# Kernel tuning notes

Measured on AMD Instinct MI355X. Metric: run time of the kernel, lower is better.

The kernel has to match this reference:

```python
import jax, jax.numpy as jnp
import numpy as np

VOCAB = 50257
EMB = 100
BOT = 5  # bottleneck dim of the tiny autoencoder MLP


def setup_inputs() -> dict:
    key = jax.random.key(0)
    ks = jax.random.split(key, 7)
    B, S = 128, 2048
    x = jax.random.randint(ks[0], (B, S), 0, VOCAB, dtype=jnp.int64)
    word_embed = jax.random.normal(ks[1], (VOCAB, EMB), dtype=jnp.float32)
    # idf values are positive; use uniform(0,1] scaled up a bit to mimic log-idf
    idf = jax.random.uniform(ks[2], (VOCAB,), dtype=jnp.float32, minval=0.01, maxval=10.0)
    fc1_w = jax.random.normal(ks[3], (BOT, EMB), dtype=jnp.float32) * (1.0 / np.sqrt(EMB))
    fc1_b = jax.random.normal(ks[4], (BOT,), dtype=jnp.float32) * 0.01
    fc2_w = jax.random.normal(ks[5], (EMB, BOT), dtype=jnp.float32) * (1.0 / np.sqrt(BOT))
    fc2_b = jax.random.normal(ks[6], (EMB,), dtype=jnp.float32) * 0.01
    return {"x": x, "word_embed": word_embed, "idf": idf,
            "fc1_w": fc1_w, "fc1_b": fc1_b, "fc2_w": fc2_w, "fc2_b": fc2_b}


def reference(x, word_embed, idf, fc1_w, fc1_b, fc2_w, fc2_b):
    B, S = x.shape
    V = idf.shape[0]
    # tf(): per-row token histogram. Equivalent math to the torch dense
    # one-hot scatter + sum over seq, done as a scatter-add (no (B,S,V) tensor).
    rows = jnp.broadcast_to(jnp.arange(B)[:, None], (B, S))
    tf = jnp.zeros((B, V), dtype=jnp.float32).at[rows, x].add(1.0)
    # tf-idf weights, row-normalized
    tfidf = tf * idf[None, :]
    tfidf = tfidf / jnp.sum(tfidf, axis=1, keepdims=True)
    # per-token weight: gather each row's tfidf at its token ids  -> [B, S]
    w = jnp.take_along_axis(tfidf, x, axis=1)
    # embedding lookup and tfidf-weighted sum over seq  -> [B, EMB]
    emb = word_embed[x]  # [B, S, EMB]
    doc = jnp.einsum('bse,bs->be', emb, w)
    # tiny 100 -> 5 -> 100 MLP (no nonlinearity in the original)
    h = doc @ fc1_w.T + fc1_b
    out = h @ fc2_w.T + fc2_b
    return out
```

## Files before the change

### kernel.cpp

```cpp
#include <hip/hip_runtime.h>

#define SEQ 2048
#define EMB 100
#define BOT 5
#define HSIZE 4096
#define SPLIT 16
#define CHUNK (SEQ / SPLIT)
#define K1T 1024

__global__ __launch_bounds__(K1T) void k1_hist(
    const int* __restrict__ x, const float* __restrict__ idf,
    float* __restrict__ coef)
{
    __shared__ int   hkey[HSIZE];
    __shared__ int   hcnt[HSIZE];
    __shared__ float red[K1T / 64];
    __shared__ float zinv;

    const int b = blockIdx.x, tid = threadIdx.x;
    const int lane = tid & 63, wid = tid >> 6;

    for (int i = tid; i < HSIZE; i += K1T) { hkey[i] = -1; hcnt[i] = 0; }
    __syncthreads();

    const int* xrow = x + (size_t)b * SEQ;

    int   mykey[SEQ / K1T];
    float myidf[SEQ / K1T];
    float z = 0.0f;
    #pragma unroll
    for (int j = 0; j < SEQ / K1T; ++j) {
        int s   = tid + j * K1T;
        int key = xrow[s];
        float w = idf[key];
        mykey[j] = key;
        myidf[j] = w;
        z += w;
        unsigned slot = ((unsigned)key * 2654435761u) >> 20;
        for (;;) {
            int prev = atomicCAS(&hkey[slot], -1, key);
            if (prev == -1 || prev == key) { atomicAdd(&hcnt[slot], 1); break; }
            slot = (slot + 1) & (HSIZE - 1);
        }
    }
    for (int off = 32; off > 0; off >>= 1) z += __shfl_down(z, off);
    if (lane == 0) red[wid] = z;
    __syncthreads();
    if (tid == 0) {
        float t = 0.0f;
        #pragma unroll
        for (int i = 0; i < K1T / 64; ++i) t += red[i];
        zinv = 1.0f / t;
    }
    __syncthreads();
    const float iz = zinv;

    #pragma unroll
    for (int j = 0; j < SEQ / K1T; ++j) {
        int s   = tid + j * K1T;
        int key = mykey[j];
        unsigned slot = ((unsigned)key * 2654435761u) >> 20;
        while (hkey[slot] != key) slot = (slot + 1) & (HSIZE - 1);
        coef[(size_t)b * SEQ + s] = (float)hcnt[slot] * myidf[j] * iz;
    }
}

__global__ __launch_bounds__(256) void k2_gather(
    const int* __restrict__ x, const float* __restrict__ coef,
    const float* __restrict__ we, float* __restrict__ partial)
{
    __shared__ int   skey[CHUNK];
    __shared__ float scoef[CHUNK];
    __shared__ float part[4][EMB];

    const int bx   = blockIdx.x;
    const int b    = bx >> 4;
    const int sp   = bx & (SPLIT - 1);
    const int tid  = threadIdx.x;
    const int wave = tid >> 6;
    const int lane = tid & 63;

    const int base = sp * CHUNK;
    if (tid < CHUNK) {
        skey [tid] = x   [(size_t)b * SEQ + base + tid];
        scoef[tid] = coef[(size_t)b * SEQ + base + tid];
    }
    __syncthreads();

    if (lane < EMB / 2) {
        float2 a0 = {0,0}, a1 = {0,0}, a2 = {0,0}, a3 = {0,0};
        float2 a4 = {0,0}, a5 = {0,0}, a6 = {0,0}, a7 = {0,0};
        const int t0 = wave * 32;
        #pragma unroll
        for (int it = 0; it < 4; ++it) {
            const int i = t0 + it * 8;
            int   k0 = skey[i+0], k1 = skey[i+1], k2 = skey[i+2], k3 = skey[i+3];
            int   k4 = skey[i+4], k5 = skey[i+5], k6 = skey[i+6], k7 = skey[i+7];
            float c0 = scoef[i+0], c1 = scoef[i+1], c2 = scoef[i+2], c3 = scoef[i+3];
            float c4 = scoef[i+4], c5 = scoef[i+5], c6 = scoef[i+6], c7 = scoef[i+7];
            float2 v0 = ((const float2*)(we + (size_t)k0 * EMB))[lane];
            float2 v1 = ((const float2*)(we + (size_t)k1 * EMB))[lane];
            float2 v2 = ((const float2*)(we + (size_t)k2 * EMB))[lane];
            float2 v3 = ((const float2*)(we + (size_t)k3 * EMB))[lane];
            float2 v4 = ((const float2*)(we + (size_t)k4 * EMB))[lane];
            float2 v5 = ((const float2*)(we + (size_t)k5 * EMB))[lane];
            float2 v6 = ((const float2*)(we + (size_t)k6 * EMB))[lane];
            float2 v7 = ((const float2*)(we + (size_t)k7 * EMB))[lane];
            a0.x += c0 * v0.x; a0.y += c0 * v0.y;
            a1.x += c1 * v1.x; a1.y += c1 * v1.y;
            a2.x += c2 * v2.x; a2.y += c2 * v2.y;
            a3.x += c3 * v3.x; a3.y += c3 * v3.y;
            a4.x += c4 * v4.x; a4.y += c4 * v4.y;
            a5.x += c5 * v5.x; a5.y += c5 * v5.y;
            a6.x += c6 * v6.x; a6.y += c6 * v6.y;
            a7.x += c7 * v7.x; a7.y += c7 * v7.y;
        }
        float sx = ((a0.x + a1.x) + (a2.x + a3.x)) + ((a4.x + a5.x) + (a6.x + a7.x));
        float sy = ((a0.y + a1.y) + (a2.y + a3.y)) + ((a4.y + a5.y) + (a6.y + a7.y));
        part[wave][2 * lane]     = sx;
        part[wave][2 * lane + 1] = sy;
    }
    __syncthreads();
    if (tid < EMB)
        partial[(size_t)bx * EMB + tid] =
            (part[0][tid] + part[1][tid]) + (part[2][tid] + part[3][tid]);
}

__global__ __launch_bounds__(128) void k3_mlp(
    const float* __restrict__ partial,
    const float* __restrict__ fc1w, const float* __restrict__ fc1b,
    const float* __restrict__ fc2w, const float* __restrict__ fc2b,
    float* __restrict__ out)
{
    __shared__ float doc[EMB];
    __shared__ float hsh[BOT];

    const int b = blockIdx.x, tid = threadIdx.x;

    if (tid < EMB) {
        float a = 0.0f;
        const float* p = partial + (size_t)b * SPLIT * EMB + tid;
        #pragma unroll
        for (int s = 0; s < SPLIT; ++s) a += p[s * EMB];
        doc[tid] = a;
    }
    __syncthreads();

    if (tid < BOT) {
        float h = fc1b[tid];
        const float* wr = fc1w + tid * EMB;
        for (int e = 0; e < EMB; ++e) h += doc[e] * wr[e];
        hsh[tid] = h;
    }
    __syncthreads();

    if (tid < EMB) {
        float o = fc2b[tid];
        const float* wr = fc2w + tid * BOT;
        #pragma unroll
        for (int j = 0; j < BOT; ++j) o += hsh[j] * wr[j];
        out[(size_t)b * EMB + tid] = o;
    }
}

extern "C" void kernel_launch(void* const* d_in, const int* in_sizes, int n_in,
                              void* d_out, int out_size, void* d_ws, size_t ws_size,
                              hipStream_t stream) {
    const int*   x    = (const int*)d_in[0];
    const float* we   = (const float*)d_in[1];
    const float* idf  = (const float*)d_in[2];
    const float* fc1w = (const float*)d_in[3];
    const float* fc1b = (const float*)d_in[4];
    const float* fc2w = (const float*)d_in[5];
    const float* fc2b = (const float*)d_in[6];
    float*       out  = (float*)d_out;

    const int B = in_sizes[0] / SEQ;

    char* ws = (char*)d_ws;
    float* coef    = (float*)ws;
    float* partial = (float*)(ws + (size_t)B * SEQ * 4);

    k1_hist  <<<B,         K1T, 0, stream>>>(x, idf, coef);
    k2_gather<<<B * SPLIT, 256, 0, stream>>>(x, coef, we, partial);
    k3_mlp   <<<B,         128, 0, stream>>>(partial, fc1w, fc1b, fc2w, fc2b, out);
}
```

Baseline: 103.3 us.

## Fuse MLP into gather via last-block counter; cache hash slots

Removes the third kernel launch. The last of the split blocks for each batch row, detected with an atomic counter that the histogram kernel resets, now reduces the partial sums and runs the small MLP. The histogram kernel also keeps the probed hash slot per token in registers, so it no longer re-probes the table in its second pass. The fusion adds thread fences and an atomic per block in exchange for one fewer launch and no inter-kernel gap.

New measurement: 349.2 us. 3.38x slower.

```diff
diff --git a/kernel.cpp b/kernel.cpp
--- a/kernel.cpp
+++ b/kernel.cpp
@@ -10,7 +10,7 @@
 
 __global__ __launch_bounds__(K1T) void k1_hist(
     const int* __restrict__ x, const float* __restrict__ idf,
-    float* __restrict__ coef)
+    float* __restrict__ coef, int* __restrict__ cnt)
 {
     __shared__ int   hkey[HSIZE];
     __shared__ int   hcnt[HSIZE];
@@ -20,12 +20,13 @@
     const int b = blockIdx.x, tid = threadIdx.x;
     const int lane = tid & 63, wid = tid >> 6;
 
+    if (tid == 0) cnt[b] = 0;
     for (int i = tid; i < HSIZE; i += K1T) { hkey[i] = -1; hcnt[i] = 0; }
     __syncthreads();
 
     const int* xrow = x + (size_t)b * SEQ;
 
-    int   mykey[SEQ / K1T];
+    int   myslot[SEQ / K1T];
     float myidf[SEQ / K1T];
     float z = 0.0f;
     #pragma unroll
@@ -33,7 +34,6 @@
         int s   = tid + j * K1T;
         int key = xrow[s];
         float w = idf[key];
-        mykey[j] = key;
         myidf[j] = w;
         z += w;
         unsigned slot = ((unsigned)key * 2654435761u) >> 20;
@@ -42,6 +42,7 @@
             if (prev == -1 || prev == key) { atomicAdd(&hcnt[slot], 1); break; }
             slot = (slot + 1) & (HSIZE - 1);
         }
+        myslot[j] = slot;
     }
     for (int off = 32; off > 0; off >>= 1) z += __shfl_down(z, off);
     if (lane == 0) red[wid] = z;
@@ -57,21 +58,25 @@
 
     #pragma unroll
     for (int j = 0; j < SEQ / K1T; ++j) {
-        int s   = tid + j * K1T;
-        int key = mykey[j];
-        unsigned slot = ((unsigned)key * 2654435761u) >> 20;
-        while (hkey[slot] != key) slot = (slot + 1) & (HSIZE - 1);
-        coef[(size_t)b * SEQ + s] = (float)hcnt[slot] * myidf[j] * iz;
+        int s = tid + j * K1T;
+        coef[(size_t)b * SEQ + s] = (float)hcnt[myslot[j]] * myidf[j] * iz;
     }
 }
 
-__global__ __launch_bounds__(256) void k2_gather(
+__global__ __launch_bounds__(256) void k2_fused(
     const int* __restrict__ x, const float* __restrict__ coef,
-    const float* __restrict__ we, float* __restrict__ partial)
+    const float* __restrict__ we, float* __restrict__ partial,
+    int* __restrict__ cnt,
+    const float* __restrict__ fc1w, const float* __restrict__ fc1b,
+    const float* __restrict__ fc2w, const float* __restrict__ fc2b,
+    float* __restrict__ out)
 {
     __shared__ int   skey[CHUNK];
     __shared__ float scoef[CHUNK];
     __shared__ float part[4][EMB];
+    __shared__ float doc[EMB];
+    __shared__ float hsh[BOT];
+    __shared__ int   slast;
 
     const int bx   = blockIdx.x;
     const int b    = bx >> 4;
@@ -80,10 +85,9 @@
     const int wave = tid >> 6;
     const int lane = tid & 63;
 
-    const int base = sp * CHUNK;
     if (tid < CHUNK) {
-        skey [tid] = x   [(size_t)b * SEQ + base + tid];
-        scoef[tid] = coef[(size_t)b * SEQ + base + tid];
+        skey [tid] = x   [(size_t)b * SEQ + sp * CHUNK + tid];
+        scoef[tid] = coef[(size_t)b * SEQ + sp * CHUNK + tid];
     }
     __syncthreads();
 
@@ -124,18 +128,13 @@
     if (tid < EMB)
         partial[(size_t)bx * EMB + tid] =
             (part[0][tid] + part[1][tid]) + (part[2][tid] + part[3][tid]);
-}
 
-__global__ __launch_bounds__(128) void k3_mlp(
-    const float* __restrict__ partial,
-    const float* __restrict__ fc1w, const float* __restrict__ fc1b,
-    const float* __restrict__ fc2w, const float* __restrict__ fc2b,
-    float* __restrict__ out)
-{
-    __shared__ float doc[EMB];
-    __shared__ float hsh[BOT];
-
-    const int b = blockIdx.x, tid = threadIdx.x;
+    __threadfence();
+    __syncthreads();
+    if (tid == 0) slast = (atomicAdd(&cnt[b], 1) == SPLIT - 1) ? 1 : 0;
+    __syncthreads();
+    if (!slast) return;
+    __threadfence();
 
     if (tid < EMB) {
         float a = 0.0f;
@@ -180,8 +179,10 @@
     char* ws = (char*)d_ws;
     float* coef    = (float*)ws;
     float* partial = (float*)(ws + (size_t)B * SEQ * 4);
+    int*   cnt     = (int*)(ws + (size_t)B * SEQ * 4
+                               + (size_t)B * SPLIT * EMB * 4);
 
-    k1_hist  <<<B,         K1T, 0, stream>>>(x, idf, coef);
-    k2_gather<<<B * SPLIT, 256, 0, stream>>>(x, coef, we, partial);
-    k3_mlp   <<<B,         128, 0, stream>>>(partial, fc1w, fc1b, fc2w, fc2b, out);
+    k1_hist <<<B,         K1T, 0, stream>>>(x, idf, coef, cnt);
+    k2_fused<<<B * SPLIT, 256, 0, stream>>>(x, coef, we, partial, cnt,
+                                            fc1w, fc1b, fc2w, fc2b, out);
 }
```

## Fuse histogram and embedding gather into one kernel with redundant per-half histograms

Applied to the files above, without the earlier changes.

Merges the tf-idf histogram kernel and the embedding gather kernel into a single kernel. Each batch row gets two blocks, and each block rebuilds the full row histogram and then gathers only its half of the sequence. This removes the coef round-trip through global memory and one kernel launch. In exchange the histogram work is done twice, and the gather runs on 256 large 1024-thread blocks instead of 2048 small ones, which may lower occupancy and parallelism.

After: 97.84 us. -5.3%, faster.

```diff
diff --git a/kernel.cpp b/kernel.cpp
--- a/kernel.cpp
+++ b/kernel.cpp
@@ -4,108 +4,88 @@
 #define EMB 100
 #define BOT 5
 #define HSIZE 4096
-#define SPLIT 16
-#define CHUNK (SEQ / SPLIT)
-#define K1T 1024
+#define RSPLIT 2
+#define HALFN (SEQ / RSPLIT)
+#define FT 1024
 
-__global__ __launch_bounds__(K1T) void k1_hist(
+__global__ __launch_bounds__(FT) void kA_fused(
     const int* __restrict__ x, const float* __restrict__ idf,
-    float* __restrict__ coef)
+    const float* __restrict__ we, float* __restrict__ partial)
 {
     __shared__ int   hkey[HSIZE];
     __shared__ int   hcnt[HSIZE];
-    __shared__ float red[K1T / 64];
+    __shared__ int   skey[SEQ];
+    __shared__ float scoef[HALFN];
+    __shared__ float part[FT / 64][EMB];
+    __shared__ float red[FT / 64];
     __shared__ float zinv;
 
-    const int b = blockIdx.x, tid = threadIdx.x;
+    const int bx   = blockIdx.x;
+    const int b    = bx >> 1;
+    const int half = bx & 1;
+    const int tid  = threadIdx.x;
     const int lane = tid & 63, wid = tid >> 6;
 
-    for (int i = tid; i < HSIZE; i += K1T) { hkey[i] = -1; hcnt[i] = 0; }
+    for (int i = tid; i < HSIZE; i += FT) { hkey[i] = -1; hcnt[i] = 0; }
+    for (int i = tid; i < SEQ; i += FT) skey[i] = x[(size_t)b * SEQ + i];
     __syncthreads();
 
-    const int* xrow = x + (size_t)b * SEQ;
+    const int k0 = skey[tid], k1 = skey[tid + FT];
+    const float w0 = idf[k0], w1 = idf[k1];
+    float z = w0 + w1;
 
-    int   mykey[SEQ / K1T];
-    float myidf[SEQ / K1T];
-    float z = 0.0f;
-    #pragma unroll
-    for (int j = 0; j < SEQ / K1T; ++j) {
-        int s   = tid + j * K1T;
-        int key = xrow[s];
-        float w = idf[key];
-        mykey[j] = key;
-        myidf[j] = w;
-        z += w;
-        unsigned slot = ((unsigned)key * 2654435761u) >> 20;
-        for (;;) {
-            int prev = atomicCAS(&hkey[slot], -1, key);
-            if (prev == -1 || prev == key) { atomicAdd(&hcnt[slot], 1); break; }
-            slot = (slot + 1) & (HSIZE - 1);
-        }
+    unsigned slot0 = ((unsigned)k0 * 2654435761u) >> 20;
+    for (;;) {
+        int prev = atomicCAS(&hkey[slot0], -1, k0);
+        if (prev == -1 || prev == k0) { atomicAdd(&hcnt[slot0], 1); break; }
+        slot0 = (slot0 + 1) & (HSIZE - 1);
     }
+    unsigned slot1 = ((unsigned)k1 * 2654435761u) >> 20;
+    for (;;) {
+        int prev = atomicCAS(&hkey[slot1], -1, k1);
+        if (prev == -1 || prev == k1) { atomicAdd(&hcnt[slot1], 1); break; }
+        slot1 = (slot1 + 1) & (HSIZE - 1);
+    }
+
     for (int off = 32; off > 0; off >>= 1) z += __shfl_down(z, off);
     if (lane == 0) red[wid] = z;
     __syncthreads();
     if (tid == 0) {
         float t = 0.0f;
         #pragma unroll
-        for (int i = 0; i < K1T / 64; ++i) t += red[i];
+        for (int i = 0; i < FT / 64; ++i) t += red[i];
         zinv = 1.0f / t;
     }
     __syncthreads();
     const float iz = zinv;
 
-    #pragma unroll
-    for (int j = 0; j < SEQ / K1T; ++j) {
-        int s   = tid + j * K1T;
-        int key = mykey[j];
-        unsigned slot = ((unsigned)key * 2654435761u) >> 20;
-        while (hkey[slot] != key) slot = (slot + 1) & (HSIZE - 1);
-        coef[(size_t)b * SEQ + s] = (float)hcnt[slot] * myidf[j] * iz;
-    }
-}
-
-__global__ __launch_bounds__(256) void k2_gather(
-    const int* __restrict__ x, const float* __restrict__ coef,
-    const float* __restrict__ we, float* __restrict__ partial)
-{
-    __shared__ int   skey[CHUNK];
-    __shared__ float scoef[CHUNK];
-    __shared__ float part[4][EMB];
-
-    const int bx   = blockIdx.x;
-    const int b    = bx >> 4;
-    const int sp   = bx & (SPLIT - 1);
-    const int tid  = threadIdx.x;
-    const int wave = tid >> 6;
-    const int lane = tid & 63;
-
-    const int base = sp * CHUNK;
-    if (tid < CHUNK) {
-        skey [tid] = x   [(size_t)b * SEQ + base + tid];
-        scoef[tid] = coef[(size_t)b * SEQ + base + tid];
+    {
+        const int      myslot = half ? (int)slot1 : (int)slot0;
+        const float    myw    = half ? w1 : w0;
+        scoef[tid] = (float)hcnt[myslot] * myw * iz;
     }
     __syncthreads();
 
     if (lane < EMB / 2) {
         float2 a0 = {0,0}, a1 = {0,0}, a2 = {0,0}, a3 = {0,0};
         float2 a4 = {0,0}, a5 = {0,0}, a6 = {0,0}, a7 = {0,0};
-        const int t0 = wave * 32;
+        const int base = half * HALFN + wid * 64;
+        const int cb   = wid * 64;
         #pragma unroll
-        for (int it = 0; it < 4; ++it) {
-            const int i = t0 + it * 8;
-            int   k0 = skey[i+0], k1 = skey[i+1], k2 = skey[i+2], k3 = skey[i+3];
-            int   k4 = skey[i+4], k5 = skey[i+5], k6 = skey[i+6], k7 = skey[i+7];
-            float c0 = scoef[i+0], c1 = scoef[i+1], c2 = scoef[i+2], c3 = scoef[i+3];
-            float c4 = scoef[i+4], c5 = scoef[i+5], c6 = scoef[i+6], c7 = scoef[i+7];
-            float2 v0 = ((const float2*)(we + (size_t)k0 * EMB))[lane];
-            float2 v1 = ((const float2*)(we + (size_t)k1 * EMB))[lane];
-            float2 v2 = ((const float2*)(we + (size_t)k2 * EMB))[lane];
-            float2 v3 = ((const float2*)(we + (size_t)k3 * EMB))[lane];
-            float2 v4 = ((const float2*)(we + (size_t)k4 * EMB))[lane];
-            float2 v5 = ((const float2*)(we + (size_t)k5 * EMB))[lane];
-            float2 v6 = ((const float2*)(we + (size_t)k6 * EMB))[lane];
-            float2 v7 = ((const float2*)(we + (size_t)k7 * EMB))[lane];
+        for (int it = 0; it < 8; ++it) {
+            const int i = it * 8;
+            int   t0 = skey[base+i+0], t1 = skey[base+i+1], t2 = skey[base+i+2], t3 = skey[base+i+3];
+            int   t4 = skey[base+i+4], t5 = skey[base+i+5], t6 = skey[base+i+6], t7 = skey[base+i+7];
+            float c0 = scoef[cb+i+0], c1 = scoef[cb+i+1], c2 = scoef[cb+i+2], c3 = scoef[cb+i+3];
+            float c4 = scoef[cb+i+4], c5 = scoef[cb+i+5], c6 = scoef[cb+i+6], c7 = scoef[cb+i+7];
+            float2 v0 = ((const float2*)(we + (size_t)t0 * EMB))[lane];
+            float2 v1 = ((const float2*)(we + (size_t)t1 * EMB))[lane];
+            float2 v2 = ((const float2*)(we + (size_t)t2 * EMB))[lane];
+            float2 v3 = ((const float2*)(we + (size_t)t3 * EMB))[lane];
+            float2 v4 = ((const float2*)(we + (size_t)t4 * EMB))[lane];
+            float2 v5 = ((const float2*)(we + (size_t)t5 * EMB))[lane];
+            float2 v6 = ((const float2*)(we + (size_t)t6 * EMB))[lane];
+            float2 v7 = ((const float2*)(we + (size_t)t7 * EMB))[lane];
             a0.x += c0 * v0.x; a0.y += c0 * v0.y;
             a1.x += c1 * v1.x; a1.y += c1 * v1.y;
             a2.x += c2 * v2.x; a2.y += c2 * v2.y;
@@ -117,16 +97,19 @@
         }
         float sx = ((a0.x + a1.x) + (a2.x + a3.x)) + ((a4.x + a5.x) + (a6.x + a7.x));
         float sy = ((a0.y + a1.y) + (a2.y + a3.y)) + ((a4.y + a5.y) + (a6.y + a7.y));
-        part[wave][2 * lane]     = sx;
-        part[wave][2 * lane + 1] = sy;
+        part[wid][2 * lane]     = sx;
+        part[wid][2 * lane + 1] = sy;
     }
     __syncthreads();
-    if (tid < EMB)
-        partial[(size_t)bx * EMB + tid] =
-            (part[0][tid] + part[1][tid]) + (part[2][tid] + part[3][tid]);
+    if (tid < EMB) {
+        float a = 0.0f;
+        #pragma unroll
+        for (int w = 0; w < FT / 64; ++w) a += part[w][tid];
+        partial[(size_t)bx * EMB + tid] = a;
+    }
 }
 
-__global__ __launch_bounds__(128) void k3_mlp(
+__global__ __launch_bounds__(128) void kB_mlp(
     const float* __restrict__ partial,
     const float* __restrict__ fc1w, const float* __restrict__ fc1b,
     const float* __restrict__ fc2w, const float* __restrict__ fc2b,
@@ -138,11 +121,8 @@
     const int b = blockIdx.x, tid = threadIdx.x;
 
     if (tid < EMB) {
-        float a = 0.0f;
-        const float* p = partial + (size_t)b * SPLIT * EMB + tid;
-        #pragma unroll
-        for (int s = 0; s < SPLIT; ++s) a += p[s * EMB];
-        doc[tid] = a;
+        const float* p = partial + (size_t)b * RSPLIT * EMB + tid;
+        doc[tid] = p[0] + p[EMB];
     }
     __syncthreads();
 
@@ -177,11 +157,8 @@
 
     const int B = in_sizes[0] / SEQ;
 
-    char* ws = (char*)d_ws;
-    float* coef    = (float*)ws;
-    float* partial = (float*)(ws + (size_t)B * SEQ * 4);
+    float* partial = (float*)d_ws;
 
-    k1_hist  <<<B,         K1T, 0, stream>>>(x, idf, coef);
-    k2_gather<<<B * SPLIT, 256, 0, stream>>>(x, coef, we, partial);
-    k3_mlp   <<<B,         128, 0, stream>>>(partial, fc1w, fc1b, fc2w, fc2b, out);
+    kA_fused<<<B * RSPLIT, FT,  0, stream>>>(x, idf, we, partial);
+    kB_mlp  <<<B,          128, 0, stream>>>(partial, fc1w, fc1b, fc2w, fc2b, out);
 }
```
